# Performance work log

Hardware: AMD Instinct MI355X
Metric: run time of the kernel (lower is better)

Reference implementation:

```python
import math
import jax, jax.numpy as jnp
import numpy as np

H, C, PQ, PV = 8, 256, 8, 12   # no_heads, c_hidden, no_qk_points, no_v_points
INF, EPS = 1e5, 1e-8

def quat_to_rot(q):
    w, x, y, z = q[..., 0], q[..., 1], q[..., 2], q[..., 3]
    r = jnp.stack([
        1 - 2*(y*y + z*z), 2*(x*y - w*z),     2*(x*z + w*y),
        2*(x*y + w*z),     1 - 2*(x*x + z*z), 2*(y*z - w*x),
        2*(x*z - w*y),     2*(y*z + w*x),     1 - 2*(x*x + y*y),
    ], axis=-1)
    return r.reshape(q.shape[:-1] + (3, 3))

def setup_inputs() -> dict:
    key = jax.random.key(0)
    ks = jax.random.split(key, 16)
    B, N, CS, CZ = 1, 512, 384, 128
    s = jax.random.normal(ks[0], (B, N, CS), jnp.float32)
    z = jax.random.normal(ks[1], (B, N, N, CZ), jnp.float32) * 0.1
    quat = jax.random.normal(ks[2], (B, N, 4), jnp.float32)
    quat = quat / jnp.linalg.norm(quat, axis=-1, keepdims=True)
    rot = quat_to_rot(quat)                       # [B,N,3,3] valid rotations
    trans = jax.random.normal(ks[3], (B, N, 3), jnp.float32) * 10.0
    mask = jnp.ones((B, N), jnp.float32)
    g = lambda k, sh: jax.random.normal(k, sh, jnp.float32) * 0.02
    params = dict(
        wq=g(ks[4], (CS, H*C)), bq=jnp.zeros((H*C,), jnp.float32),
        wkv=g(ks[5], (CS, 2*H*C)), bkv=jnp.zeros((2*H*C,), jnp.float32),
        wqp=g(ks[6], (CS, H*PQ*3)), bqp=jnp.zeros((H*PQ*3,), jnp.float32),
        wkvp=g(ks[7], (CS, H*(PQ+PV)*3)), bkvp=jnp.zeros((H*(PQ+PV)*3,), jnp.float32),
        wb=g(ks[8], (CZ, H)), bb=jnp.zeros((H,), jnp.float32),
        wz=g(ks[9], (CZ, CZ//4)), bz=jnp.zeros((CZ//4,), jnp.float32),
        head_weights=jnp.full((H,), 0.541324854612918, jnp.float32),  # softplus^-1(1)
        wo=g(ks[10], (H*(C + 4*PV + CZ//4), CS)), bo=jnp.zeros((CS,), jnp.float32),
    )
    return dict(s=s, z=z, rot=rot, trans=trans, mask=mask, **params)

def reference(s, z, rot, trans, mask, wq, bq, wkv, bkv, wqp, bqp, wkvp, bkvp, wb, bb, wz, bz, head_weights, wo, bo):
    B, N, CS = s.shape
    q = (s @ wq + bq).reshape(B, N, H, C)
    kv = (s @ wkv + bkv).reshape(B, N, H, 2 * C)
    k, v = kv[..., :C], kv[..., C:]

    def split_pts(x):  # torch split-into-3 + stack(-1): [B,N,3*M] -> [B,N,M,3]
        return jnp.moveaxis(x.reshape(B, N, 3, -1), -2, -1)

    def apply_rigid(p):  # global frame: R @ p + t
        return jnp.einsum('bnij,bnpj->bnpi', rot, p) + trans[:, :, None, :]

    q_pts = apply_rigid(split_pts(s @ wqp + bqp)).reshape(B, N, H, PQ, 3)
    kv_pts = apply_rigid(split_pts(s @ wkvp + bkvp)).reshape(B, N, H, PQ + PV, 3)
    k_pts, v_pts = kv_pts[..., :PQ, :], kv_pts[..., PQ:, :]

    b_bias = z @ wb + bb                                  # [B,Ni,Nj,H]
    a = jnp.einsum('bihc,bjhc->bhij', q, k) * math.sqrt(1.0 / (3 * C))
    a = a + math.sqrt(1.0 / 3) * jnp.moveaxis(b_bias, -1, 1)

    disp = q_pts[:, :, None] - k_pts[:, None]             # [B,Ni,Nj,H,PQ,3]
    pt_att = jnp.sum(disp * disp, axis=-1)                # [B,Ni,Nj,H,PQ]
    hw = jax.nn.softplus(head_weights) * math.sqrt(1.0 / (3 * (PQ * 9.0 / 2)))
    pt_att = -0.5 * jnp.sum(pt_att * hw[None, None, None, :, None], axis=-1)  # [B,Ni,Nj,H]

    sq_mask = INF * (mask[:, :, None] * mask[:, None, :] - 1.0)
    a = a + jnp.moveaxis(pt_att, -1, 1) + sq_mask[:, None]
    a = jax.nn.softmax(a, axis=-1)                        # [B,H,Ni,Nj]

    o = jnp.einsum('bhij,bjhc->bihc', a, v).reshape(B, N, H * C)

    o_pt = jnp.einsum('bhij,bjhpd->bihpd', a, v_pts)      # [B,N,H,PV,3] global
    o_pt = jnp.einsum('bnji,bnhpj->bnhpi', rot, o_pt - trans[:, :, None, None, :])  # invert_apply
    o_pt_norm = jnp.sqrt(jnp.sum(o_pt * o_pt, axis=-1) + EPS).reshape(B, N, H * PV)
    o_pt_flat = o_pt.reshape(B, N, H * PV, 3)

    pair_z = z @ wz + bz                                  # [B,Ni,Nj,CZ//4]
    o_pair = jnp.einsum('bhij,bijd->bihd', a, pair_z).reshape(B, N, -1)

    feats = jnp.concatenate(
        [o, o_pt_flat[..., 0], o_pt_flat[..., 1], o_pt_flat[..., 2], o_pt_norm, o_pair], axis=-1)
    return feats @ wo + bo
```

## Files before the change

### kernel.cpp

```cpp
#include <hip/hip_runtime.h>


#define OFF_QBH    0
#define OFF_KBH    524288
#define OFF_VB     1048576
#define OFF_QPRAW  2097152
#define OFF_KVPRAW 2195456
#define OFF_QPTS   2441216
#define OFF_KVPTS  2539520
#define OFF_BBIAS  2785280
#define OFF_PAIRZT 3833856
#define OFF_ATTNH  8028160
#define OFF_FEATSB 9076736
#define OFF_WCAT   9764864
#define OFF_WTALL  9767936
#define OFF_VPT    11082752
#define OFF_WOT    11803648
#define OFF_QPTH   12319744
#define OFF_QPTL   12385280
#define OFF_KPTH   12450816
#define OFF_KPTL   12516352
#define OFF_QP2    12581888
#define OFF_KP2    12585984
#define OFF_SBF    12590080

typedef __attribute__((ext_vector_type(8))) short short8;
typedef __attribute__((ext_vector_type(4))) float f32x4;

__device__ __forceinline__ unsigned short f2bf(float f) {
  union { float f; unsigned u; } v; v.f = f;
  unsigned u = v.u;
  unsigned r = (u + 0x7fffu + ((u >> 16) & 1u)) >> 16;
  return (unsigned short)r;
}
__device__ __forceinline__ float bf2f(unsigned short h) {
  union { unsigned u; float f; } v; v.u = ((unsigned)h) << 16; return v.f;
}
__device__ __forceinline__ short8 pack8(float4 a, float4 b) {
  short8 r;
  r[0] = (short)f2bf(a.x); r[1] = (short)f2bf(a.y);
  r[2] = (short)f2bf(a.z); r[3] = (short)f2bf(a.w);
  r[4] = (short)f2bf(b.x); r[5] = (short)f2bf(b.y);
  r[6] = (short)f2bf(b.z); r[7] = (short)f2bf(b.w);
  return r;
}

__global__ __launch_bounds__(256) void prep_all(
    const float* __restrict__ wq, const float* __restrict__ wkv,
    const float* __restrict__ wqp, const float* __restrict__ wkvp,
    const float* __restrict__ wo, const float* __restrict__ wb,
    const float* __restrict__ wz, const float* __restrict__ s,
    unsigned short* __restrict__ wTall, unsigned short* __restrict__ woT,
    unsigned short* __restrict__ wT, unsigned short* __restrict__ sbf) {
  __shared__ float tile[64][65];
  const int b = blockIdx.x, t = threadIdx.x;
  if (b < 642) {
    const int ntile = b % 107, kt = b / 107;
    const float* src; int Nsrc, nloc0;
    const int ng0 = ntile * 64;
    if (ntile < 32)      { src = wq;   Nsrc = 2048; nloc0 = ng0; }
    else if (ntile < 96) { src = wkv;  Nsrc = 4096; nloc0 = ng0 - 2048; }
    else if (ntile < 99) { src = wqp;  Nsrc = 192;  nloc0 = ng0 - 6144; }
    else                 { src = wkvp; Nsrc = 480;  nloc0 = ng0 - 6336; }
    const int r = t >> 2, cs = (t & 3) * 16;
#pragma unroll
    for (int i = 0; i < 16; i += 4) {
      int n = nloc0 + cs + i;
      float4 v;
      if (n + 3 < Nsrc) v = *(const float4*)(src + (size_t)(kt * 64 + r) * Nsrc + n);
      else {
        v.x = (n + 0 < Nsrc) ? src[(size_t)(kt * 64 + r) * Nsrc + n + 0] : 0.f;
        v.y = (n + 1 < Nsrc) ? src[(size_t)(kt * 64 + r) * Nsrc + n + 1] : 0.f;
        v.z = (n + 2 < Nsrc) ? src[(size_t)(kt * 64 + r) * Nsrc + n + 2] : 0.f;
        v.w = (n + 3 < Nsrc) ? src[(size_t)(kt * 64 + r) * Nsrc + n + 3] : 0.f;
      }
      tile[r][cs + i + 0] = v.x; tile[r][cs + i + 1] = v.y;
      tile[r][cs + i + 2] = v.z; tile[r][cs + i + 3] = v.w;
    }
    __syncthreads();
    const int nr = t >> 2, ks = (t & 3) * 16;
    unsigned short ov[16];
#pragma unroll
    for (int i = 0; i < 16; i++) ov[i] = f2bf(tile[ks + i][nr]);
    unsigned short* dst = wTall + (size_t)(ng0 + nr) * 384 + kt * 64 + ks;
    *(uint4*)(dst) = *(const uint4*)&ov[0];
    *(uint4*)(dst + 8) = *(const uint4*)&ov[8];
  } else if (b < 894) {
    const int idx = b - 642;
    const int kt = idx % 42, ntile = idx / 42;
    const int r = t >> 2, cs = (t & 3) * 16;
#pragma unroll
    for (int i = 0; i < 16; i += 4) {
      float4 v = *(const float4*)(wo + (size_t)(kt * 64 + r) * 384 + ntile * 64 + cs + i);
      tile[r][cs + i + 0] = v.x; tile[r][cs + i + 1] = v.y;
      tile[r][cs + i + 2] = v.z; tile[r][cs + i + 3] = v.w;
    }
    __syncthreads();
    const int nr = t >> 2, ks = (t & 3) * 16;
    unsigned short ov[16];
#pragma unroll
    for (int i = 0; i < 16; i++) ov[i] = f2bf(tile[ks + i][nr]);
    unsigned short* dst = woT + (size_t)(ntile * 64 + nr) * 2688 + kt * 64 + ks;
    *(uint4*)(dst) = *(const uint4*)&ov[0];
    *(uint4*)(dst + 8) = *(const uint4*)&ov[8];
  } else if (b < 918) {
    const int l = (b - 894) * 256 + t;
    if (l < 6144) {
      int n = l >> 7, k = l & 127;
      float v = (n < 8) ? wb[k * 8 + n] * 0.5773502691896258f
                        : (n < 40 ? wz[k * 32 + (n - 8)] : 0.f);
      wT[l] = f2bf(v);
    }
  } else {
    const int gid = (b - 918) * 256 + t;
    const int off = gid * 8;
    float4 a0 = *(const float4*)(s + off);
    float4 a1 = *(const float4*)(s + off + 4);
    *(short8*)(sbf + off) = pack8(a0, a1);
  }
}

__global__ __launch_bounds__(256) void proj_mfma(
    const unsigned short* __restrict__ sbf, const unsigned short* __restrict__ wTall,
    const float* __restrict__ bq, const float* __restrict__ bkv,
    const float* __restrict__ bqp, const float* __restrict__ bkvp,
    unsigned short* __restrict__ qbh, unsigned short* __restrict__ kbh,
    float* __restrict__ vb, float* __restrict__ qpraw, float* __restrict__ kvpraw) {
  const int bx = blockIdx.x, row0 = blockIdx.y * 64;
  const int lane = threadIdx.x & 63, wv = threadIdx.x >> 6;
  const int quad = lane >> 4, m = lane & 15;
  const int n0 = bx * 64;
  const unsigned short* srow = sbf + (size_t)(row0 + wv * 16 + m) * 384;
  f32x4 acc[4];
#pragma unroll
  for (int nt = 0; nt < 4; nt++) acc[nt] = (f32x4){0.f, 0.f, 0.f, 0.f};

#pragma unroll
  for (int ksx = 0; ksx < 12; ksx++) {
    const int c0 = ksx * 32 + quad * 8;
    short8 af = *(const short8*)(srow + c0);
#pragma unroll
    for (int nt = 0; nt < 4; nt++) {
      short8 bf = *(const short8*)(wTall + (size_t)(n0 + nt * 16 + m) * 384 + c0);
      acc[nt] = __builtin_amdgcn_mfma_f32_16x16x32_bf16(af, bf, acc[nt], 0, 0, 0);
    }
  }

  const int rbase = row0 + wv * 16 + quad * 4;
#pragma unroll
  for (int nt = 0; nt < 4; nt++) {
    const int col = n0 + nt * 16 + m;
    if (n0 < 2048) {
      const float bias = bq[col];
#pragma unroll
      for (int r = 0; r < 4; r++)
        qbh[(size_t)(rbase + r) * 2048 + col] = f2bf(acc[nt][r] + bias);
    } else if (n0 < 6144) {
      const int ckv = col - 2048;
      const float bias = bkv[ckv];
      const int hh = ckv >> 9, c = ckv & 511;
      if (c < 256) {
#pragma unroll
        for (int r = 0; r < 4; r++)
          kbh[(size_t)(rbase + r) * 2048 + hh * 256 + c] = f2bf(acc[nt][r] + bias);
      } else {
#pragma unroll
        for (int r = 0; r < 4; r++)
          vb[(size_t)(rbase + r) * 2048 + hh * 256 + (c - 256)] = acc[nt][r] + bias;
      }
    } else if (n0 < 6336) {
      const int cq = col - 6144;
      const float bias = bqp[cq];
#pragma unroll
      for (int r = 0; r < 4; r++)
        qpraw[(size_t)(rbase + r) * 192 + cq] = acc[nt][r] + bias;
    } else {
      const int ck = col - 6336;
      if (ck < 480) {
        const float bias = bkvp[ck];
#pragma unroll
        for (int r = 0; r < 4; r++)
          kvpraw[(size_t)(rbase + r) * 480 + ck] = acc[nt][r] + bias;
      }
    }
  }
}

__global__ __launch_bounds__(256) void rigid_pts(
    const float* __restrict__ qpraw, const float* __restrict__ kvpraw,
    const float* __restrict__ rot, const float* __restrict__ trans,
    float* __restrict__ qpts, float* __restrict__ kvpts) {
  int gid = blockIdx.x * 256 + threadIdx.x;
  int n = gid / 224, r = gid % 224;
  const float* R  = rot + n * 9;
  const float* tr = trans + n * 3;
  float px, py, pz; float* dst;
  if (r < 64) {
    const float* src = qpraw + (size_t)n * 192;
    px = src[r]; py = src[64 + r]; pz = src[128 + r];
    dst = qpts + ((size_t)n * 64 + r) * 3;
  } else {
    int p = r - 64;
    const float* src = kvpraw + (size_t)n * 480;
    px = src[p]; py = src[160 + p]; pz = src[320 + p];
    dst = kvpts + ((size_t)n * 160 + p) * 3;
  }
  dst[0] = R[0] * px + R[1] * py + R[2] * pz + tr[0];
  dst[1] = R[3] * px + R[4] * py + R[5] * pz + tr[1];
  dst[2] = R[6] * px + R[7] * py + R[8] * pz + tr[2];
}

__global__ __launch_bounds__(256) void pts_planes(
    const float* __restrict__ qpts, const float* __restrict__ kvpts,
    unsigned short* __restrict__ qptH, unsigned short* __restrict__ qptL,
    unsigned short* __restrict__ kptH, unsigned short* __restrict__ kptL,
    float* __restrict__ qp2g, float* __restrict__ kp2g) {
  const int row = blockIdx.x * 256 + threadIdx.x;
  const int h = blockIdx.y;
  {
    const float* src = qpts + ((size_t)row * 64 + h * 8) * 3;
    unsigned short hi[32], lo[32]; float s2 = 0.f;
#pragma unroll
    for (int w = 0; w < 24; w++) {
      float x = src[w];
      hi[w] = f2bf(x); lo[w] = f2bf(x - bf2f(hi[w]));
      s2 += x * x;
    }
#pragma unroll
    for (int w = 24; w < 32; w++) { hi[w] = 0; lo[w] = 0; }
    unsigned short* dh = qptH + ((size_t)h * 512 + row) * 32;
    unsigned short* dl = qptL + ((size_t)h * 512 + row) * 32;
#pragma unroll
    for (int g = 0; g < 4; g++) {
      *(uint4*)(dh + g * 8) = *(const uint4*)&hi[g * 8];
      *(uint4*)(dl + g * 8) = *(const uint4*)&lo[g * 8];
    }
    qp2g[h * 512 + row] = s2;
  }
  {
    const float* src = kvpts + ((size_t)row * 160 + h * 20) * 3;
    unsigned short hi[32], lo[32]; float s2 = 0.f;
#pragma unroll
    for (int w = 0; w < 24; w++) {
      float x = src[w];
      hi[w] = f2bf(x); lo[w] = f2bf(x - bf2f(hi[w]));
      s2 += x * x;
    }
#pragma unroll
    for (int w = 24; w < 32; w++) { hi[w] = 0; lo[w] = 0; }
    unsigned short* dh = kptH + ((size_t)h * 512 + row) * 32;
    unsigned short* dl = kptL + ((size_t)h * 512 + row) * 32;
#pragma unroll
    for (int g = 0; g < 4; g++) {
      *(uint4*)(dh + g * 8) = *(const uint4*)&hi[g * 8];
      *(uint4*)(dl + g * 8) = *(const uint4*)&lo[g * 8];
    }
    kp2g[h * 512 + row] = s2;
  }
}

__global__ __launch_bounds__(256) void zpass_mfma(
    const float* __restrict__ z, const unsigned short* __restrict__ wT,
    const float* __restrict__ bb, const float* __restrict__ bz,
    unsigned short* __restrict__ bbias_tb, unsigned short* __restrict__ pairzT) {
  __shared__ __align__(16) unsigned short lb[4][8][16];
  __shared__ __align__(16) unsigned short lp[4][32][16];
  const int lane = threadIdx.x & 63;
  const int wave = threadIdx.x >> 6;
  const int quad = lane >> 4, m = lane & 15;
  const int tile = blockIdx.x * 4 + wave;
  const int row0 = tile * 16;

  short8 bf[3][4];
#pragma unroll
  for (int nt = 0; nt < 3; nt++)
#pragma unroll
    for (int s = 0; s < 4; s++)
      bf[nt][s] = *(const short8*)(wT + (size_t)(nt * 16 + m) * 128 + s * 32 + quad * 8);

  float bias[3];
#pragma unroll
  for (int nt = 0; nt < 3; nt++) {
    int c = nt * 16 + m;
    bias[nt] = (c < 8) ? 0.5773502691896258f * bb[c] : (c < 40 ? bz[c - 8] : 0.f);
  }

  f32x4 acc[3];
#pragma unroll
  for (int nt = 0; nt < 3; nt++) acc[nt] = (f32x4){0.f, 0.f, 0.f, 0.f};

  const float* zr = z + (size_t)(row0 + m) * 128 + quad * 8;
#pragma unroll
  for (int s = 0; s < 4; s++) {
    float4 a0 = *(const float4*)(zr + s * 32);
    float4 a1 = *(const float4*)(zr + s * 32 + 4);
    short8 af = pack8(a0, a1);
#pragma unroll
    for (int nt = 0; nt < 3; nt++)
      acc[nt] = __builtin_amdgcn_mfma_f32_16x16x32_bf16(af, bf[nt][s], acc[nt], 0, 0, 0);
  }

#pragma unroll
  for (int nt = 0; nt < 3; nt++) {
    const int c = nt * 16 + m;
#pragma unroll
    for (int r = 0; r < 4; r++) {
      const float v = acc[nt][r] + bias[nt];
      const int jl = quad * 4 + r;
      if (c < 8)       lb[wave][c][jl] = f2bf(v);
      else if (c < 40) lp[wave][c - 8][jl] = f2bf(v);
    }
  }
  const int i = row0 >> 9, j0 = row0 & 511;
  if (lane < 16) {
    int c = lane >> 1, half = lane & 1;
    uint4 val = *(const uint4*)&lb[wave][c][half * 8];
    *(uint4*)(bbias_tb + (size_t)c * 262144 + row0 + half * 8) = val;
  }
  {
    int d = lane >> 1, half = lane & 1;
    uint4 val = *(const uint4*)&lp[wave][d][half * 8];
    *(uint4*)(pairzT + ((size_t)i * 32 + d) * 512 + j0 + half * 8) = val;
  }
}

__global__ __launch_bounds__(256) void vpt_prep(
    const float* __restrict__ vb, const float* __restrict__ kvpts,
    unsigned short* __restrict__ vptT) {
  const int jt = blockIdx.x, h = blockIdx.y, part = blockIdx.z;
  const int j0 = jt * 64, t = threadIdx.x;
  if (part < 4) {
    __shared__ float tile[64][65];
    const int c0 = part * 64;
    const int r = t >> 2, cs = (t & 3) * 16;
#pragma unroll
    for (int ii = 0; ii < 16; ii += 4) {
      float4 v = *(const float4*)(vb + (size_t)(j0 + r) * 2048 + h * 256 + c0 + cs + ii);
      tile[r][cs + ii + 0] = v.x; tile[r][cs + ii + 1] = v.y;
      tile[r][cs + ii + 2] = v.z; tile[r][cs + ii + 3] = v.w;
    }
    __syncthreads();
    const int cl = t >> 2, js = (t & 3) * 16;
    unsigned short ov[16];
#pragma unroll
    for (int x = 0; x < 16; x++) ov[x] = f2bf(tile[js + x][cl]);
    unsigned short* dst = vptT + ((size_t)h * 352 + c0 + cl) * 512 + j0 + js;
    *(uint4*)dst = *(const uint4*)&ov[0];
    *(uint4*)(dst + 8) = *(const uint4*)&ov[8];
  } else {
    __shared__ float lds[64][37];
    for (int l = t; l < 64 * 36; l += 256) {
      int jl = l / 36, w = l % 36;
      lds[jl][w] = kvpts[((size_t)(j0 + jl) * 160 + h * 20 + 8) * 3 + w];
    }
    __syncthreads();
#pragma unroll
    for (int step = 0; step < 3; step++) {
      int chunk = t + 256 * step;
      int row = chunk >> 3, js = (chunk & 7) * 8;
      unsigned short ov[8];
#pragma unroll
      for (int x = 0; x < 8; x++) {
        int w = (row < 48) ? row : row - 48;
        float f = (w < 36) ? lds[js + x][w] : 0.f;
        unsigned short hi = f2bf(f);
        ov[x] = (row < 48) ? hi : f2bf(f - bf2f(hi));
      }
      *(uint4*)(vptT + ((size_t)h * 352 + 256 + row) * 512 + j0 + js) = *(const uint4*)&ov[0];
    }
  }
}

__global__ __launch_bounds__(512) void logits_fused(
    const unsigned short* __restrict__ qbh, const unsigned short* __restrict__ kbh,
    const unsigned short* __restrict__ qptH, const unsigned short* __restrict__ qptL,
    const unsigned short* __restrict__ kptH, const unsigned short* __restrict__ kptL,
    const float* __restrict__ qp2g, const float* __restrict__ kp2g,
    const unsigned short* __restrict__ bbias_tb, const float* __restrict__ mask,
    const float* __restrict__ hwp, const unsigned short* __restrict__ vptT,
    const float* __restrict__ rot, const float* __restrict__ trans,
    unsigned short* __restrict__ attnh, unsigned short* __restrict__ featsb) {
  const int it = blockIdx.x, h = blockIdx.y;
  const int i0 = it * 16;
  __shared__ __align__(16) unsigned short sth[8][16][72], stl[8][16][72];
  __shared__ float redm[16][8], reds[16][8];
  __shared__ float lds_h[16][48], lds_l[16][48];
  const int t = threadIdx.x;
  const int lane = t & 63, wv = t >> 6;
  const int quad = lane >> 4, m = lane & 15;
  const int jw0 = wv * 64;

  f32x4 acc[4];
#pragma unroll
  for (int nt = 0; nt < 4; nt++) acc[nt] = (f32x4){0.f, 0.f, 0.f, 0.f};
  const unsigned short* qrow = qbh + (size_t)(i0 + m) * 2048 + h * 256;
#pragma unroll
  for (int s = 0; s < 8; s++) {
    short8 af = *(const short8*)(qrow + s * 32 + quad * 8);
#pragma unroll
    for (int nt = 0; nt < 4; nt++) {
      short8 bfr = *(const short8*)(kbh + (size_t)(jw0 + nt * 16 + m) * 2048 + h * 256 + s * 32 + quad * 8);
      acc[nt] = __builtin_amdgcn_mfma_f32_16x16x32_bf16(af, bfr, acc[nt], 0, 0, 0);
    }
  }

  short8 aqh = *(const short8*)(qptH + ((size_t)h * 512 + i0 + m) * 32 + quad * 8);
  short8 aql = *(const short8*)(qptL + ((size_t)h * 512 + i0 + m) * 32 + quad * 8);
  f32x4 accp[4];
#pragma unroll
  for (int nt = 0; nt < 4; nt++) {
    const size_t krow = ((size_t)h * 512 + jw0 + nt * 16 + m) * 32 + quad * 8;
    short8 bkh = *(const short8*)(kptH + krow);
    short8 bkl = *(const short8*)(kptL + krow);
    f32x4 p = (f32x4){0.f, 0.f, 0.f, 0.f};
    p = __builtin_amdgcn_mfma_f32_16x16x32_bf16(aqh, bkh, p, 0, 0, 0);
    p = __builtin_amdgcn_mfma_f32_16x16x32_bf16(aqh, bkl, p, 0, 0, 0);
    p = __builtin_amdgcn_mfma_f32_16x16x32_bf16(aql, bkh, p, 0, 0, 0);
    accp[nt] = p;
  }

  const float c1 = 0.03608439182435161f;
  const float hw = log1pf(expf(hwp[h])) * 0.09622504486493764f;
  float qp2v[4];
#pragma unroll
  for (int r = 0; r < 4; r++) qp2v[r] = qp2g[h * 512 + i0 + quad * 4 + r];
  float lg[4][4];
  float rmax[4] = {-1e30f, -1e30f, -1e30f, -1e30f};
#pragma unroll
  for (int nt = 0; nt < 4; nt++) {
    const int j = jw0 + nt * 16 + m;
    const float kp2v = kp2g[h * 512 + j];
    const float mj = mask[j];
#pragma unroll
    for (int r = 0; r < 4; r++) {
      const int il = quad * 4 + r;
      const float pt = qp2v[r] + kp2v - 2.f * accp[nt][r];
      float v = c1 * acc[nt][r]
              + bf2f(bbias_tb[(size_t)h * 262144 + (size_t)(i0 + il) * 512 + j])
              - 0.5f * hw * pt
              + 100000.f * (mask[i0 + il] * mj - 1.f);
      lg[nt][r] = v;
      rmax[r] = fmaxf(rmax[r], v);
    }
  }
#pragma unroll
  for (int r = 0; r < 4; r++) {
#pragma unroll
    for (int off = 1; off < 16; off <<= 1) rmax[r] = fmaxf(rmax[r], __shfl_xor(rmax[r], off));
  }
  if (m == 0) {
#pragma unroll
    for (int r = 0; r < 4; r++) redm[quad * 4 + r][wv] = rmax[r];
  }
  __syncthreads();
  float rowm[4], rsum[4];
#pragma unroll
  for (int r = 0; r < 4; r++) {
    const int il = quad * 4 + r;
    float m0 = fmaxf(fmaxf(redm[il][0], redm[il][1]), fmaxf(redm[il][2], redm[il][3]));
    float m1 = fmaxf(fmaxf(redm[il][4], redm[il][5]), fmaxf(redm[il][6], redm[il][7]));
    rowm[r] = fmaxf(m0, m1);
    rsum[r] = 0.f;
  }
#pragma unroll
  for (int nt = 0; nt < 4; nt++)
#pragma unroll
    for (int r = 0; r < 4; r++) {
      float e = __expf(lg[nt][r] - rowm[r]);
      lg[nt][r] = e;
      rsum[r] += e;
    }
#pragma unroll
  for (int r = 0; r < 4; r++) {
#pragma unroll
    for (int off = 1; off < 16; off <<= 1) rsum[r] += __shfl_xor(rsum[r], off);
  }
  if (m == 0) {
#pragma unroll
    for (int r = 0; r < 4; r++) reds[quad * 4 + r][wv] = rsum[r];
  }
  __syncthreads();
  float inv[4];
#pragma unroll
  for (int r = 0; r < 4; r++) {
    const int il = quad * 4 + r;
    float s0 = (reds[il][0] + reds[il][1]) + (reds[il][2] + reds[il][3]);
    float s1 = (reds[il][4] + reds[il][5]) + (reds[il][6] + reds[il][7]);
    inv[r] = 1.f / (s0 + s1);
  }
#pragma unroll
  for (int nt = 0; nt < 4; nt++)
#pragma unroll
    for (int r = 0; r < 4; r++) {
      const int il = quad * 4 + r;
      float a = lg[nt][r] * inv[r];
      unsigned short hi = f2bf(a);
      sth[wv][il][nt * 16 + m] = hi;
      stl[wv][il][nt * 16 + m] = f2bf(a - bf2f(hi));
    }
  __syncthreads();
#pragma unroll
  for (int step = 0; step < 2; step++) {
    const int idx = lane + 64 * step;
    const int il = idx >> 3, seg = idx & 7;
    uint4 vh = *(const uint4*)&sth[wv][il][seg * 8];
    *(uint4*)(attnh + ((size_t)h * 512 + i0 + il) * 512 + jw0 + seg * 8) = vh;
  }

  const int nt0 = (wv < 6) ? wv * 3 : 18 + (wv - 6) * 2;
  const int ncnt = (wv < 6) ? 3 : 2;
  f32x4 vacc[3];
#pragma unroll
  for (int k = 0; k < 3; k++) vacc[k] = (f32x4){0.f, 0.f, 0.f, 0.f};
  const unsigned short* vbase = vptT + (size_t)h * 352 * 512;
#pragma unroll
  for (int s = 0; s < 16; s++) {
    const int wsrc = s >> 1, col = (s & 1) * 32 + quad * 8;
    short8 ah = *(const short8*)&sth[wsrc][m][col];
    short8 al = *(const short8*)&stl[wsrc][m][col];
    const int ko = s * 32 + quad * 8;
#pragma unroll
    for (int k = 0; k < 3; k++) {
      if (k < ncnt) {
        const int nt = nt0 + k;
        short8 bfr = *(const short8*)(vbase + (size_t)(nt * 16 + m) * 512 + ko);
        vacc[k] = __builtin_amdgcn_mfma_f32_16x16x32_bf16(ah, bfr, vacc[k], 0, 0, 0);
        if (nt >= 16 && nt < 19)
          vacc[k] = __builtin_amdgcn_mfma_f32_16x16x32_bf16(al, bfr, vacc[k], 0, 0, 0);
      }
    }
  }
#pragma unroll
  for (int k = 0; k < 3; k++) {
    if (k < ncnt) {
      const int nt = nt0 + k;
      if (nt < 16) {
#pragma unroll
        for (int r = 0; r < 4; r++)
          featsb[(size_t)(i0 + quad * 4 + r) * 2688 + h * 256 + nt * 16 + m] = f2bf(vacc[k][r]);
      } else if (nt < 19) {
        const int w = (nt - 16) * 16 + m;
#pragma unroll
        for (int r = 0; r < 4; r++) if (w < 36) lds_h[quad * 4 + r][w] = vacc[k][r];
      } else {
        const int w = (nt - 19) * 16 + m;
#pragma unroll
        for (int r = 0; r < 4; r++) if (w < 36) lds_l[quad * 4 + r][w] = vacc[k][r];
      }
    }
  }
  __syncthreads();
  if (t < 192) {
    const int il = t / 12, p = t % 12, irow = i0 + il;
    const float* R = rot + irow * 9;
    const float* tr = trans + irow * 3;
    float x  = lds_h[il][p * 3 + 0] + lds_l[il][p * 3 + 0] - tr[0];
    float y  = lds_h[il][p * 3 + 1] + lds_l[il][p * 3 + 1] - tr[1];
    float zz = lds_h[il][p * 3 + 2] + lds_l[il][p * 3 + 2] - tr[2];
    float o0 = R[0] * x + R[3] * y + R[6] * zz;
    float o1 = R[1] * x + R[4] * y + R[7] * zz;
    float o2 = R[2] * x + R[5] * y + R[8] * zz;
    float nrm = sqrtf(o0 * o0 + o1 * o1 + o2 * o2 + 1e-8f);
    unsigned short* fr = featsb + (size_t)irow * 2688 + 2048;
    fr[h * 12 + p]       = f2bf(o0);
    fr[96 + h * 12 + p]  = f2bf(o1);
    fr[192 + h * 12 + p] = f2bf(o2);
    fr[288 + h * 12 + p] = f2bf(nrm);
  }
}

__global__ __launch_bounds__(256) void o_pair_mfma(
    const unsigned short* __restrict__ attnh, const unsigned short* __restrict__ pairzT,
    unsigned short* __restrict__ featsb) {
  const int lane = threadIdx.x & 63, wv = threadIdx.x >> 6;
  const int quad = lane >> 4, m = lane & 15;
  const int i = blockIdx.x * 4 + wv;
  f32x4 acc[2];
  acc[0] = (f32x4){0.f, 0.f, 0.f, 0.f};
  acc[1] = (f32x4){0.f, 0.f, 0.f, 0.f};
#pragma unroll
  for (int s = 0; s < 16; s++) {
    const int ko = s * 32 + quad * 8;
    short8 af = *(const short8*)(attnh + (size_t)(m & 7) * 262144 + (size_t)i * 512 + ko);
#pragma unroll
    for (int nt = 0; nt < 2; nt++) {
      short8 bfr = *(const short8*)(pairzT + ((size_t)i * 32 + nt * 16 + m) * 512 + ko);
      acc[nt] = __builtin_amdgcn_mfma_f32_16x16x32_bf16(af, bfr, acc[nt], 0, 0, 0);
    }
  }
  if (quad < 2) {
#pragma unroll
    for (int nt = 0; nt < 2; nt++)
#pragma unroll
      for (int r = 0; r < 4; r++) {
        const int hh = quad * 4 + r, d = nt * 16 + m;
        featsb[(size_t)i * 2688 + 2432 + hh * 32 + d] = f2bf(acc[nt][r]);
      }
  }
}

__global__ __launch_bounds__(256) void out_mfma(
    const unsigned short* __restrict__ featsb, const unsigned short* __restrict__ woT,
    const float* __restrict__ bo, float* __restrict__ out) {
  const int it = blockIdx.x, ng = blockIdx.y;
  const int lane = threadIdx.x & 63, wv = threadIdx.x >> 6;
  const int quad = lane >> 4, m = lane & 15;
  const int i0 = it * 16, n0 = (ng * 4 + wv) * 16;
  const unsigned short* arow = featsb + (size_t)(i0 + m) * 2688;
  const unsigned short* brow = woT + (size_t)(n0 + m) * 2688;
  f32x4 acc = (f32x4){0.f, 0.f, 0.f, 0.f};
#pragma unroll 4
  for (int s = 0; s < 84; s++) {
    const int ko = s * 32 + quad * 8;
    short8 af = *(const short8*)(arow + ko);
    short8 bf = *(const short8*)(brow + ko);
    acc = __builtin_amdgcn_mfma_f32_16x16x32_bf16(af, bf, acc, 0, 0, 0);
  }
  const float bias = bo[n0 + m];
#pragma unroll
  for (int r = 0; r < 4; r++)
    out[(size_t)(i0 + quad * 4 + r) * 384 + n0 + m] = acc[r] + bias;
}

extern "C" void kernel_launch(void* const* d_in, const int* in_sizes, int n_in,
                              void* d_out, int out_size, void* d_ws, size_t ws_size,
                              hipStream_t stream) {
  const float* s     = (const float*)d_in[0];
  const float* z     = (const float*)d_in[1];
  const float* rot   = (const float*)d_in[2];
  const float* trans = (const float*)d_in[3];
  const float* mask  = (const float*)d_in[4];
  const float* wq    = (const float*)d_in[5];
  const float* bq    = (const float*)d_in[6];
  const float* wkv   = (const float*)d_in[7];
  const float* bkv   = (const float*)d_in[8];
  const float* wqp   = (const float*)d_in[9];
  const float* bqp   = (const float*)d_in[10];
  const float* wkvp  = (const float*)d_in[11];
  const float* bkvp  = (const float*)d_in[12];
  const float* wb    = (const float*)d_in[13];
  const float* bb    = (const float*)d_in[14];
  const float* wz    = (const float*)d_in[15];
  const float* bz    = (const float*)d_in[16];
  const float* hwp   = (const float*)d_in[17];
  const float* wo    = (const float*)d_in[18];
  const float* bo    = (const float*)d_in[19];
  float* out = (float*)d_out;

  float* ws = (float*)d_ws;
  unsigned short* qbh   = (unsigned short*)(ws + OFF_QBH);
  unsigned short* kbh   = (unsigned short*)(ws + OFF_KBH);
  float* vb      = ws + OFF_VB;
  float* qpraw   = ws + OFF_QPRAW;
  float* kvpraw  = ws + OFF_KVPRAW;
  float* qpts    = ws + OFF_QPTS;
  float* kvpts   = ws + OFF_KVPTS;
  unsigned short* bbias_tb = (unsigned short*)(ws + OFF_BBIAS);
  unsigned short* pairzT   = (unsigned short*)(ws + OFF_PAIRZT);
  unsigned short* attnh    = (unsigned short*)(ws + OFF_ATTNH);
  unsigned short* featsb   = (unsigned short*)(ws + OFF_FEATSB);
  unsigned short* wT    = (unsigned short*)(ws + OFF_WCAT);
  unsigned short* wTall = (unsigned short*)(ws + OFF_WTALL);
  unsigned short* vptT  = (unsigned short*)(ws + OFF_VPT);
  unsigned short* woT   = (unsigned short*)(ws + OFF_WOT);
  unsigned short* qptH  = (unsigned short*)(ws + OFF_QPTH);
  unsigned short* qptL  = (unsigned short*)(ws + OFF_QPTL);
  unsigned short* kptH  = (unsigned short*)(ws + OFF_KPTH);
  unsigned short* kptL  = (unsigned short*)(ws + OFF_KPTL);
  float* qp2g = ws + OFF_QP2;
  float* kp2g = ws + OFF_KP2;
  unsigned short* sbf = (unsigned short*)(ws + OFF_SBF);

  prep_all<<<1014, 256, 0, stream>>>(wq, wkv, wqp, wkvp, wo, wb, wz, s,
                                     wTall, woT, wT, sbf);
  proj_mfma<<<dim3(107, 8), 256, 0, stream>>>(sbf, wTall, bq, bkv, bqp, bkvp,
                                              qbh, kbh, vb, qpraw, kvpraw);
  rigid_pts<<<448, 256, 0, stream>>>(qpraw, kvpraw, rot, trans, qpts, kvpts);
  pts_planes<<<dim3(2, 8), 256, 0, stream>>>(qpts, kvpts, qptH, qptL, kptH, kptL, qp2g, kp2g);
  zpass_mfma<<<4096, 256, 0, stream>>>(z, wT, bb, bz, bbias_tb, pairzT);
  vpt_prep<<<dim3(8, 8, 5), 256, 0, stream>>>(vb, kvpts, vptT);
  logits_fused<<<dim3(32, 8), 512, 0, stream>>>(qbh, kbh, qptH, qptL, kptH, kptL,
                                                qp2g, kp2g, bbias_tb, mask, hwp,
                                                vptT, rot, trans, attnh, featsb);
  o_pair_mfma<<<128, 256, 0, stream>>>(attnh, pairzT, featsb);
  out_mfma<<<dim3(32, 6), 256, 0, stream>>>(featsb, woT, bo, out);
}
```

Measured before the change: 352.0 us.

## Merge projection, z-pass and point-prep kernels into two combined launches

Combines the z-pair projection and the s projection GEMM into a single launch, split by block index. The rigid transform, point-plane split and v-point transpose are merged into a second launch that applies the rotation inline, so the intermediate qpts/kvpts buffers are no longer written or read. The goal is to cut launch count and inter-kernel gaps and to let the two independent GEMMs run concurrently. The cost is some duplicated rotation work in the v-point path, plus branch divergence and shared-memory reuse across the block roles.

```diff
diff --git a/kernel.cpp b/kernel.cpp
--- a/kernel.cpp
+++ b/kernel.cpp
@@ -6,8 +6,6 @@
 #define OFF_VB     1048576
 #define OFF_QPRAW  2097152
 #define OFF_KVPRAW 2195456
-#define OFF_QPTS   2441216
-#define OFF_KVPTS  2539520
 #define OFF_BBIAS  2785280
 #define OFF_PAIRZT 3833856
 #define OFF_ATTNH  8028160
@@ -120,253 +118,242 @@
   }
 }
 
-__global__ __launch_bounds__(256) void proj_mfma(
+__global__ __launch_bounds__(256) void mega1(
+    const float* __restrict__ z, const unsigned short* __restrict__ wT,
+    const float* __restrict__ bb, const float* __restrict__ bz,
+    unsigned short* __restrict__ bbias_tb, unsigned short* __restrict__ pairzT,
     const unsigned short* __restrict__ sbf, const unsigned short* __restrict__ wTall,
     const float* __restrict__ bq, const float* __restrict__ bkv,
     const float* __restrict__ bqp, const float* __restrict__ bkvp,
     unsigned short* __restrict__ qbh, unsigned short* __restrict__ kbh,
     float* __restrict__ vb, float* __restrict__ qpraw, float* __restrict__ kvpraw) {
-  const int bx = blockIdx.x, row0 = blockIdx.y * 64;
+  __shared__ __align__(16) unsigned short lb[4][8][16];
+  __shared__ __align__(16) unsigned short lp[4][32][16];
   const int lane = threadIdx.x & 63, wv = threadIdx.x >> 6;
   const int quad = lane >> 4, m = lane & 15;
-  const int n0 = bx * 64;
-  const unsigned short* srow = sbf + (size_t)(row0 + wv * 16 + m) * 384;
-  f32x4 acc[4];
-#pragma unroll
-  for (int nt = 0; nt < 4; nt++) acc[nt] = (f32x4){0.f, 0.f, 0.f, 0.f};
-
-#pragma unroll
-  for (int ksx = 0; ksx < 12; ksx++) {
-    const int c0 = ksx * 32 + quad * 8;
-    short8 af = *(const short8*)(srow + c0);
+  if (blockIdx.x < 4096) {
+    const int tile = blockIdx.x * 4 + wv;
+    const int row0 = tile * 16;
+    short8 bf[3][4];
+#pragma unroll
+    for (int nt = 0; nt < 3; nt++)
+#pragma unroll
+      for (int s = 0; s < 4; s++)
+        bf[nt][s] = *(const short8*)(wT + (size_t)(nt * 16 + m) * 128 + s * 32 + quad * 8);
+    float bias[3];
+#pragma unroll
+    for (int nt = 0; nt < 3; nt++) {
+      int c = nt * 16 + m;
+      bias[nt] = (c < 8) ? 0.5773502691896258f * bb[c] : (c < 40 ? bz[c - 8] : 0.f);
+    }
+    f32x4 acc[3];
+#pragma unroll
+    for (int nt = 0; nt < 3; nt++) acc[nt] = (f32x4){0.f, 0.f, 0.f, 0.f};
+    const float* zr = z + (size_t)(row0 + m) * 128 + quad * 8;
+#pragma unroll
+    for (int s = 0; s < 4; s++) {
+      float4 a0 = *(const float4*)(zr + s * 32);
+      float4 a1 = *(const float4*)(zr + s * 32 + 4);
+      short8 af = pack8(a0, a1);
+#pragma unroll
+      for (int nt = 0; nt < 3; nt++)
+        acc[nt] = __builtin_amdgcn_mfma_f32_16x16x32_bf16(af, bf[nt][s], acc[nt], 0, 0, 0);
+    }
+#pragma unroll
+    for (int nt = 0; nt < 3; nt++) {
+      const int c = nt * 16 + m;
+#pragma unroll
+      for (int r = 0; r < 4; r++) {
+        const float v = acc[nt][r] + bias[nt];
+        const int jl = quad * 4 + r;
+        if (c < 8)       lb[wv][c][jl] = f2bf(v);
+        else if (c < 40) lp[wv][c - 8][jl] = f2bf(v);
+      }
+    }
+    const int i = row0 >> 9, j0 = row0 & 511;
+    if (lane < 16) {
+      int c = lane >> 1, half = lane & 1;
+      uint4 val = *(const uint4*)&lb[wv][c][half * 8];
+      *(uint4*)(bbias_tb + (size_t)c * 262144 + row0 + half * 8) = val;
+    }
+    {
+      int d = lane >> 1, half = lane & 1;
+      uint4 val = *(const uint4*)&lp[wv][d][half * 8];
+      *(uint4*)(pairzT + ((size_t)i * 32 + d) * 512 + j0 + half * 8) = val;
+    }
+  } else {
+    const int b2 = blockIdx.x - 4096;
+    const int bx = b2 % 107, row0 = (b2 / 107) * 64;
+    const int n0 = bx * 64;
+    const unsigned short* srow = sbf + (size_t)(row0 + wv * 16 + m) * 384;
+    f32x4 acc[4];
+#pragma unroll
+    for (int nt = 0; nt < 4; nt++) acc[nt] = (f32x4){0.f, 0.f, 0.f, 0.f};
+#pragma unroll
+    for (int ksx = 0; ksx < 12; ksx++) {
+      const int c0 = ksx * 32 + quad * 8;
+      short8 af = *(const short8*)(srow + c0);
+#pragma unroll
+      for (int nt = 0; nt < 4; nt++) {
+        short8 bfw = *(const short8*)(wTall + (size_t)(n0 + nt * 16 + m) * 384 + c0);
+        acc[nt] = __builtin_amdgcn_mfma_f32_16x16x32_bf16(af, bfw, acc[nt], 0, 0, 0);
+      }
+    }
+    const int rbase = row0 + wv * 16 + quad * 4;
 #pragma unroll
     for (int nt = 0; nt < 4; nt++) {
-      short8 bf = *(const short8*)(wTall + (size_t)(n0 + nt * 16 + m) * 384 + c0);
-      acc[nt] = __builtin_amdgcn_mfma_f32_16x16x32_bf16(af, bf, acc[nt], 0, 0, 0);
-    }
-  }
-
-  const int rbase = row0 + wv * 16 + quad * 4;
-#pragma unroll
-  for (int nt = 0; nt < 4; nt++) {
-    const int col = n0 + nt * 16 + m;
-    if (n0 < 2048) {
-      const float bias = bq[col];
-#pragma unroll
-      for (int r = 0; r < 4; r++)
-        qbh[(size_t)(rbase + r) * 2048 + col] = f2bf(acc[nt][r] + bias);
-    } else if (n0 < 6144) {
-      const int ckv = col - 2048;
-      const float bias = bkv[ckv];
-      const int hh = ckv >> 9, c = ckv & 511;
-      if (c < 256) {
+      const int col = n0 + nt * 16 + m;
+      if (n0 < 2048) {
+        const float bias = bq[col];
 #pragma unroll
         for (int r = 0; r < 4; r++)
-          kbh[(size_t)(rbase + r) * 2048 + hh * 256 + c] = f2bf(acc[nt][r] + bias);
+          qbh[(size_t)(rbase + r) * 2048 + col] = f2bf(acc[nt][r] + bias);
+      } else if (n0 < 6144) {
+        const int ckv = col - 2048;
+        const float bias = bkv[ckv];
+        const int hh = ckv >> 9, c = ckv & 511;
+        if (c < 256) {
+#pragma unroll
+          for (int r = 0; r < 4; r++)
+            kbh[(size_t)(rbase + r) * 2048 + hh * 256 + c] = f2bf(acc[nt][r] + bias);
+        } else {
+#pragma unroll
+          for (int r = 0; r < 4; r++)
+            vb[(size_t)(rbase + r) * 2048 + hh * 256 + (c - 256)] = acc[nt][r] + bias;
+        }
+      } else if (n0 < 6336) {
+        const int cq = col - 6144;
+        const float bias = bqp[cq];
+#pragma unroll
+        for (int r = 0; r < 4; r++)
+          qpraw[(size_t)(rbase + r) * 192 + cq] = acc[nt][r] + bias;
       } else {
-#pragma unroll
-        for (int r = 0; r < 4; r++)
-          vb[(size_t)(rbase + r) * 2048 + hh * 256 + (c - 256)] = acc[nt][r] + bias;
-      }
-    } else if (n0 < 6336) {
-      const int cq = col - 6144;
-      const float bias = bqp[cq];
-#pragma unroll
-      for (int r = 0; r < 4; r++)
-        qpraw[(size_t)(rbase + r) * 192 + cq] = acc[nt][r] + bias;
-    } else {
-      const int ck = col - 6336;
-      if (ck < 480) {
-        const float bias = bkvp[ck];
-#pragma unroll
-        for (int r = 0; r < 4; r++)
-          kvpraw[(size_t)(rbase + r) * 480 + ck] = acc[nt][r] + bias;
-      }
-    }
-  }
-}
-
-__global__ __launch_bounds__(256) void rigid_pts(
-    const float* __restrict__ qpraw, const float* __restrict__ kvpraw,
-    const float* __restrict__ rot, const float* __restrict__ trans,
-    float* __restrict__ qpts, float* __restrict__ kvpts) {
-  int gid = blockIdx.x * 256 + threadIdx.x;
-  int n = gid / 224, r = gid % 224;
-  const float* R  = rot + n * 9;
-  const float* tr = trans + n * 3;
-  float px, py, pz; float* dst;
-  if (r < 64) {
-    const float* src = qpraw + (size_t)n * 192;
-    px = src[r]; py = src[64 + r]; pz = src[128 + r];
-    dst = qpts + ((size_t)n * 64 + r) * 3;
-  } else {
-    int p = r - 64;
-    const float* src = kvpraw + (size_t)n * 480;
-    px = src[p]; py = src[160 + p]; pz = src[320 + p];
-    dst = kvpts + ((size_t)n * 160 + p) * 3;
-  }
-  dst[0] = R[0] * px + R[1] * py + R[2] * pz + tr[0];
-  dst[1] = R[3] * px + R[4] * py + R[5] * pz + tr[1];
-  dst[2] = R[6] * px + R[7] * py + R[8] * pz + tr[2];
-}
-
-__global__ __launch_bounds__(256) void pts_planes(
-    const float* __restrict__ qpts, const float* __restrict__ kvpts,
+        const int ck = col - 6336;
+        if (ck < 480) {
+          const float bias = bkvp[ck];
+#pragma unroll
+          for (int r = 0; r < 4; r++)
+            kvpraw[(size_t)(rbase + r) * 480 + ck] = acc[nt][r] + bias;
+        }
+      }
+    }
+  }
+}
+
+__global__ __launch_bounds__(256) void mega2(
+    const float* __restrict__ vb, const float* __restrict__ qpraw,
+    const float* __restrict__ kvpraw, const float* __restrict__ rot,
+    const float* __restrict__ trans, unsigned short* __restrict__ vptT,
     unsigned short* __restrict__ qptH, unsigned short* __restrict__ qptL,
     unsigned short* __restrict__ kptH, unsigned short* __restrict__ kptL,
     float* __restrict__ qp2g, float* __restrict__ kp2g) {
-  const int row = blockIdx.x * 256 + threadIdx.x;
-  const int h = blockIdx.y;
-  {
-    const float* src = qpts + ((size_t)row * 64 + h * 8) * 3;
-    unsigned short hi[32], lo[32]; float s2 = 0.f;
-#pragma unroll
-    for (int w = 0; w < 24; w++) {
-      float x = src[w];
-      hi[w] = f2bf(x); lo[w] = f2bf(x - bf2f(hi[w]));
-      s2 += x * x;
-    }
-#pragma unroll
-    for (int w = 24; w < 32; w++) { hi[w] = 0; lo[w] = 0; }
-    unsigned short* dh = qptH + ((size_t)h * 512 + row) * 32;
-    unsigned short* dl = qptL + ((size_t)h * 512 + row) * 32;
-#pragma unroll
-    for (int g = 0; g < 4; g++) {
-      *(uint4*)(dh + g * 8) = *(const uint4*)&hi[g * 8];
-      *(uint4*)(dl + g * 8) = *(const uint4*)&lo[g * 8];
-    }
-    qp2g[h * 512 + row] = s2;
-  }
-  {
-    const float* src = kvpts + ((size_t)row * 160 + h * 20) * 3;
-    unsigned short hi[32], lo[32]; float s2 = 0.f;
-#pragma unroll
-    for (int w = 0; w < 24; w++) {
-      float x = src[w];
-      hi[w] = f2bf(x); lo[w] = f2bf(x - bf2f(hi[w]));
-      s2 += x * x;
-    }
-#pragma unroll
-    for (int w = 24; w < 32; w++) { hi[w] = 0; lo[w] = 0; }
-    unsigned short* dh = kptH + ((size_t)h * 512 + row) * 32;
-    unsigned short* dl = kptL + ((size_t)h * 512 + row) * 32;
-#pragma unroll
-    for (int g = 0; g < 4; g++) {
-      *(uint4*)(dh + g * 8) = *(const uint4*)&hi[g * 8];
-      *(uint4*)(dl + g * 8) = *(const uint4*)&lo[g * 8];
-    }
-    kp2g[h * 512 + row] = s2;
-  }
-}
-
-__global__ __launch_bounds__(256) void zpass_mfma(
-    const float* __restrict__ z, const unsigned short* __restrict__ wT,
-    const float* __restrict__ bb, const float* __restrict__ bz,
-    unsigned short* __restrict__ bbias_tb, unsigned short* __restrict__ pairzT) {
-  __shared__ __align__(16) unsigned short lb[4][8][16];
-  __shared__ __align__(16) unsigned short lp[4][32][16];
-  const int lane = threadIdx.x & 63;
-  const int wave = threadIdx.x >> 6;
-  const int quad = lane >> 4, m = lane & 15;
-  const int tile = blockIdx.x * 4 + wave;
-  const int row0 = tile * 16;
-
-  short8 bf[3][4];
-#pragma unroll
-  for (int nt = 0; nt < 3; nt++)
-#pragma unroll
-    for (int s = 0; s < 4; s++)
-      bf[nt][s] = *(const short8*)(wT + (size_t)(nt * 16 + m) * 128 + s * 32 + quad * 8);
-
-  float bias[3];
-#pragma unroll
-  for (int nt = 0; nt < 3; nt++) {
-    int c = nt * 16 + m;
-    bias[nt] = (c < 8) ? 0.5773502691896258f * bb[c] : (c < 40 ? bz[c - 8] : 0.f);
-  }
-
-  f32x4 acc[3];
-#pragma unroll
-  for (int nt = 0; nt < 3; nt++) acc[nt] = (f32x4){0.f, 0.f, 0.f, 0.f};
-
-  const float* zr = z + (size_t)(row0 + m) * 128 + quad * 8;
-#pragma unroll
-  for (int s = 0; s < 4; s++) {
-    float4 a0 = *(const float4*)(zr + s * 32);
-    float4 a1 = *(const float4*)(zr + s * 32 + 4);
-    short8 af = pack8(a0, a1);
-#pragma unroll
-    for (int nt = 0; nt < 3; nt++)
-      acc[nt] = __builtin_amdgcn_mfma_f32_16x16x32_bf16(af, bf[nt][s], acc[nt], 0, 0, 0);
-  }
-
-#pragma unroll
-  for (int nt = 0; nt < 3; nt++) {
-    const int c = nt * 16 + m;
-#pragma unroll
-    for (int r = 0; r < 4; r++) {
-      const float v = acc[nt][r] + bias[nt];
-      const int jl = quad * 4 + r;
-      if (c < 8)       lb[wave][c][jl] = f2bf(v);
-      else if (c < 40) lp[wave][c - 8][jl] = f2bf(v);
-    }
-  }
-  const int i = row0 >> 9, j0 = row0 & 511;
-  if (lane < 16) {
-    int c = lane >> 1, half = lane & 1;
-    uint4 val = *(const uint4*)&lb[wave][c][half * 8];
-    *(uint4*)(bbias_tb + (size_t)c * 262144 + row0 + half * 8) = val;
-  }
-  {
-    int d = lane >> 1, half = lane & 1;
-    uint4 val = *(const uint4*)&lp[wave][d][half * 8];
-    *(uint4*)(pairzT + ((size_t)i * 32 + d) * 512 + j0 + half * 8) = val;
-  }
-}
-
-__global__ __launch_bounds__(256) void vpt_prep(
-    const float* __restrict__ vb, const float* __restrict__ kvpts,
-    unsigned short* __restrict__ vptT) {
-  const int jt = blockIdx.x, h = blockIdx.y, part = blockIdx.z;
-  const int j0 = jt * 64, t = threadIdx.x;
-  if (part < 4) {
-    __shared__ float tile[64][65];
-    const int c0 = part * 64;
-    const int r = t >> 2, cs = (t & 3) * 16;
-#pragma unroll
-    for (int ii = 0; ii < 16; ii += 4) {
-      float4 v = *(const float4*)(vb + (size_t)(j0 + r) * 2048 + h * 256 + c0 + cs + ii);
-      tile[r][cs + ii + 0] = v.x; tile[r][cs + ii + 1] = v.y;
-      tile[r][cs + ii + 2] = v.z; tile[r][cs + ii + 3] = v.w;
-    }
-    __syncthreads();
-    const int cl = t >> 2, js = (t & 3) * 16;
-    unsigned short ov[16];
-#pragma unroll
-    for (int x = 0; x < 16; x++) ov[x] = f2bf(tile[js + x][cl]);
-    unsigned short* dst = vptT + ((size_t)h * 352 + c0 + cl) * 512 + j0 + js;
-    *(uint4*)dst = *(const uint4*)&ov[0];
-    *(uint4*)(dst + 8) = *(const uint4*)&ov[8];
+  __shared__ float tile[64][65];
+  const int b = blockIdx.x, t = threadIdx.x;
+  if (b < 320) {
+    const int jt = b & 7, h = (b >> 3) & 7, part = b >> 6;
+    const int j0 = jt * 64;
+    if (part < 4) {
+      const int c0 = part * 64;
+      const int r = t >> 2, cs = (t & 3) * 16;
+#pragma unroll
+      for (int ii = 0; ii < 16; ii += 4) {
+        float4 v = *(const float4*)(vb + (size_t)(j0 + r) * 2048 + h * 256 + c0 + cs + ii);
+        tile[r][cs + ii + 0] = v.x; tile[r][cs + ii + 1] = v.y;
+        tile[r][cs + ii + 2] = v.z; tile[r][cs + ii + 3] = v.w;
+      }
+      __syncthreads();
+      const int cl = t >> 2, js = (t & 3) * 16;
+      unsigned short ov[16];
+#pragma unroll
+      for (int x = 0; x < 16; x++) ov[x] = f2bf(tile[js + x][cl]);
+      unsigned short* dst = vptT + ((size_t)h * 352 + c0 + cl) * 512 + j0 + js;
+      *(uint4*)dst = *(const uint4*)&ov[0];
+      *(uint4*)(dst + 8) = *(const uint4*)&ov[8];
+    } else {
+      float (*lds)[37] = (float(*)[37])&tile[0][0];
+      for (int l = t; l < 64 * 36; l += 256) {
+        int jl = l / 36, w = l % 36;
+        int p = w / 3, d = w % 3;
+        const int n = j0 + jl;
+        const int pidx = h * 20 + 8 + p;
+        const float* kr = kvpraw + (size_t)n * 480;
+        float px = kr[pidx], py = kr[160 + pidx], pz = kr[320 + pidx];
+        const float* R = rot + n * 9;
+        lds[jl][w] = R[d * 3 + 0] * px + R[d * 3 + 1] * py + R[d * 3 + 2] * pz + trans[n * 3 + d];
+      }
+      __syncthreads();
+#pragma unroll
+      for (int step = 0; step < 3; step++) {
+        int chunk = t + 256 * step;
+        int row = chunk >> 3, js = (chunk & 7) * 8;
+        unsigned short ov[8];
+#pragma unroll
+        for (int x = 0; x < 8; x++) {
+          int w = (row < 48) ? row : row - 48;
+          float f = (w < 36) ? lds[js + x][w] : 0.f;
+          unsigned short hi = f2bf(f);
+          ov[x] = (row < 48) ? hi : f2bf(f - bf2f(hi));
+        }
+        *(uint4*)(vptT + ((size_t)h * 352 + 256 + row) * 512 + j0 + js) = *(const uint4*)&ov[0];
+      }
+    }
   } else {
-    __shared__ float lds[64][37];
-    for (int l = t; l < 64 * 36; l += 256) {
-      int jl = l / 36, w = l % 36;
-      lds[jl][w] = kvpts[((size_t)(j0 + jl) * 160 + h * 20 + 8) * 3 + w];
-    }
-    __syncthreads();
-#pragma unroll
-    for (int step = 0; step < 3; step++) {
-      int chunk = t + 256 * step;
-      int row = chunk >> 3, js = (chunk & 7) * 8;
-      unsigned short ov[8];
-#pragma unroll
-      for (int x = 0; x < 8; x++) {
-        int w = (row < 48) ? row : row - 48;
-        float f = (w < 36) ? lds[js + x][w] : 0.f;
-        unsigned short hi = f2bf(f);
-        ov[x] = (row < 48) ? hi : f2bf(f - bf2f(hi));
-      }
-      *(uint4*)(vptT + ((size_t)h * 352 + 256 + row) * 512 + j0 + js) = *(const uint4*)&ov[0];
+    const int idx = b - 320;
+    const int row = (idx & 1) * 256 + t;
+    const int h = idx >> 1;
+    const float* R  = rot + row * 9;
+    const float* tr = trans + row * 3;
+    {
+      const float* qr = qpraw + (size_t)row * 192;
+      unsigned short hi[32], lo[32]; float s2 = 0.f;
+#pragma unroll
+      for (int p = 0; p < 8; p++) {
+        const int pidx = h * 8 + p;
+        float px = qr[pidx], py = qr[64 + pidx], pz = qr[128 + pidx];
+        float X = R[0] * px + R[1] * py + R[2] * pz + tr[0];
+        float Y = R[3] * px + R[4] * py + R[5] * pz + tr[1];
+        float Z = R[6] * px + R[7] * py + R[8] * pz + tr[2];
+        hi[p * 3 + 0] = f2bf(X); lo[p * 3 + 0] = f2bf(X - bf2f(hi[p * 3 + 0]));
+        hi[p * 3 + 1] = f2bf(Y); lo[p * 3 + 1] = f2bf(Y - bf2f(hi[p * 3 + 1]));
+        hi[p * 3 + 2] = f2bf(Z); lo[p * 3 + 2] = f2bf(Z - bf2f(hi[p * 3 + 2]));
+        s2 += X * X + Y * Y + Z * Z;
+      }
+#pragma unroll
+      for (int w = 24; w < 32; w++) { hi[w] = 0; lo[w] = 0; }
+      unsigned short* dh = qptH + ((size_t)h * 512 + row) * 32;
+      unsigned short* dl = qptL + ((size_t)h * 512 + row) * 32;
+#pragma unroll
+      for (int g = 0; g < 4; g++) {
+        *(uint4*)(dh + g * 8) = *(const uint4*)&hi[g * 8];
+        *(uint4*)(dl + g * 8) = *(const uint4*)&lo[g * 8];
+      }
+      qp2g[h * 512 + row] = s2;
+    }
+    {
+      const float* kr = kvpraw + (size_t)row * 480;
+      unsigned short hi[32], lo[32]; float s2 = 0.f;
+#pragma unroll
+      for (int p = 0; p < 8; p++) {
+        const int pidx = h * 20 + p;
+        float px = kr[pidx], py = kr[160 + pidx], pz = kr[320 + pidx];
+        float X = R[0] * px + R[1] * py + R[2] * pz + tr[0];
+        float Y = R[3] * px + R[4] * py + R[5] * pz + tr[1];
+        float Z = R[6] * px + R[7] * py + R[8] * pz + tr[2];
+        hi[p * 3 + 0] = f2bf(X); lo[p * 3 + 0] = f2bf(X - bf2f(hi[p * 3 + 0]));
+        hi[p * 3 + 1] = f2bf(Y); lo[p * 3 + 1] = f2bf(Y - bf2f(hi[p * 3 + 1]));
+        hi[p * 3 + 2] = f2bf(Z); lo[p * 3 + 2] = f2bf(Z - bf2f(hi[p * 3 + 2]));
+        s2 += X * X + Y * Y + Z * Z;
+      }
+#pragma unroll
+      for (int w = 24; w < 32; w++) { hi[w] = 0; lo[w] = 0; }
+      unsigned short* dh = kptH + ((size_t)h * 512 + row) * 32;
+      unsigned short* dl = kptL + ((size_t)h * 512 + row) * 32;
+#pragma unroll
+      for (int g = 0; g < 4; g++) {
+        *(uint4*)(dh + g * 8) = *(const uint4*)&hi[g * 8];
+        *(uint4*)(dl + g * 8) = *(const uint4*)&lo[g * 8];
+      }
+      kp2g[h * 512 + row] = s2;
     }
   }
 }
@@ -653,8 +640,6 @@
   float* vb      = ws + OFF_VB;
   float* qpraw   = ws + OFF_QPRAW;
   float* kvpraw  = ws + OFF_KVPRAW;
-  float* qpts    = ws + OFF_QPTS;
-  float* kvpts   = ws + OFF_KVPTS;
   unsigned short* bbias_tb = (unsigned short*)(ws + OFF_BBIAS);
   unsigned short* pairzT   = (unsigned short*)(ws + OFF_PAIRZT);
   unsigned short* attnh    = (unsigned short*)(ws + OFF_ATTNH);
@@ -673,12 +658,11 @@
 
   prep_all<<<1014, 256, 0, stream>>>(wq, wkv, wqp, wkvp, wo, wb, wz, s,
                                      wTall, woT, wT, sbf);
-  proj_mfma<<<dim3(107, 8), 256, 0, stream>>>(sbf, wTall, bq, bkv, bqp, bkvp,
-                                              qbh, kbh, vb, qpraw, kvpraw);
-  rigid_pts<<<448, 256, 0, stream>>>(qpraw, kvpraw, rot, trans, qpts, kvpts);
-  pts_planes<<<dim3(2, 8), 256, 0, stream>>>(qpts, kvpts, qptH, qptL, kptH, kptL, qp2g, kp2g);
-  zpass_mfma<<<4096, 256, 0, stream>>>(z, wT, bb, bz, bbias_tb, pairzT);
-  vpt_prep<<<dim3(8, 8, 5), 256, 0, stream>>>(vb, kvpts, vptT);
+  mega1<<<4952, 256, 0, stream>>>(z, wT, bb, bz, bbias_tb, pairzT,
+                                  sbf, wTall, bq, bkv, bqp, bkvp,
+                                  qbh, kbh, vb, qpraw, kvpraw);
+  mega2<<<336, 256, 0, stream>>>(vb, qpraw, kvpraw, rot, trans, vptT,
+                                 qptH, qptL, kptH, kptL, qp2g, kp2g);
   logits_fused<<<dim3(32, 8), 512, 0, stream>>>(qbh, kbh, qptH, qptL, kptH, kptL,
                                                 qp2g, kp2g, bbias_tb, mask, hwp,
                                                 vptT, rot, trans, attnh, featsb);
```

Result: faster. 337.6 us (-4.1%).
